# Kernel optimization log

Hardware: AMD Instinct MI355X
Metric: run time of the kernel (lower is better)

The kernel has to match this reference:

```python
import jax, jax.numpy as jnp
import numpy as np

B, P, D = 16, 512, 1024   # batch, num wordpieces, bert_dim (roberta-large)
W, T, E = 400, 32, 64     # num words, num triggers (spans), num entities (spans)
H = 600                   # hidden_num of role_idn_ffn


def _make_idxs(rng, b, m, n, max_len):
    # [start, end) intervals with 0 <= start < end <= n, sorted starts per row
    starts = np.sort(rng.integers(0, n - 1, size=(b, m)), axis=1)
    ends = np.minimum(starts + rng.integers(1, max_len + 1, size=(b, m)), n)
    ends = np.maximum(ends, starts + 1)
    return np.stack([starts, ends], axis=-1).astype(np.int32)


def setup_inputs() -> dict:
    key = jax.random.key(0)
    k1, k2, k3 = jax.random.split(key, 3)
    rng = np.random.default_rng(0)
    return {
        "piece_reprs": jax.random.normal(k1, (B, P, D), dtype=jnp.float32),
        "word_idxs": jnp.asarray(_make_idxs(rng, B, W, P, 4)),
        "trigger_idxs": jnp.asarray(_make_idxs(rng, B, T, W, 8)),
        "entity_idxs": jnp.asarray(_make_idxs(rng, B, E, W, 12)),
        "W0": jax.random.normal(k2, (4 * D, H), dtype=jnp.float32) * 0.02,
        "b0": jnp.zeros((H,), dtype=jnp.float32),
        "W1": jax.random.normal(k3, (H, 2), dtype=jnp.float32) * 0.02,
        "b1": jnp.zeros((2,), dtype=jnp.float32),
    }


def _segment_mean(x, idxs):
    """Mean of x[b, start:end] per interval. x: [B,N,Dm], idxs: [B,M,2] -> [B,M,Dm].
    Vectorized replacement of the nested-loop slice+mean via inclusive prefix sums."""
    cs = jnp.concatenate([jnp.zeros_like(x[:, :1]), jnp.cumsum(x, axis=1)], axis=1)  # [B,N+1,Dm]
    s = jnp.take_along_axis(cs, idxs[:, :, 0:1], axis=1)  # [B,M,Dm]
    e = jnp.take_along_axis(cs, idxs[:, :, 1:2], axis=1)  # [B,M,Dm]
    lens = (idxs[:, :, 1] - idxs[:, :, 0]).astype(x.dtype)[:, :, None]
    return (e - s) / lens


def reference(piece_reprs, word_idxs, trigger_idxs, entity_idxs, W0, b0, W1, b1):
    # encode(): wordpiece -> word averaging (compute_word_reps_avg)
    word_reprs = _segment_mean(piece_reprs, word_idxs)          # [B, W, D]
    # scores(): span mean pooling (compute_span_reprs)
    trig = _segment_mean(word_reprs, trigger_idxs)              # [B, T, D]
    ent = _segment_mean(word_reprs, entity_idxs)                # [B, E, D]
    b, t, d = trig.shape
    e = ent.shape[1]
    # compute_binary_reprs: all (trigger, entity) pairs, trigger index varies slowly
    t_rep = jnp.broadcast_to(trig[:, :, None, :], (b, t, e, d)).reshape(b, t * e, d)
    e_rep = jnp.broadcast_to(ent[:, None, :, :], (b, t, e, d)).reshape(b, t * e, d)
    role = jnp.concatenate([t_rep, e_rep, t_rep * e_rep, jnp.abs(t_rep - e_rep)], axis=-1)  # [B,T*E,4D]
    # role_idn_ffn: Linears([4D, H, 2]) with relu between layers (dropout=0 at eval)
    h = jax.nn.relu(role @ W0 + b0)
    return h @ W1 + b1                                          # [B, T*E, 2]
```

## Files before the change

### kernel.cpp

```cpp
#include <hip/hip_runtime.h>
#include <cstddef>
#include <cstdint>

typedef float f32x4 __attribute__((ext_vector_type(4)));
typedef __bf16 bf16x8 __attribute__((ext_vector_type(8)));

constexpr int NB = 16;
constexpr int NP = 512;
constexpr int ND = 1024;
constexpr int NW = 400;
constexpr int NT = 32;
constexpr int NE = 64;
constexpr int NH = 600;
constexpr int IMGP = 128 * 64;
constexpr int IMGQ = 320 * 32;

__device__ inline bf16x8 pack8(float a0, float a1, float a2, float a3,
                               float a4, float a5, float a6, float a7) {
    bf16x8 v;
    v[0] = (__bf16)a0; v[1] = (__bf16)a1; v[2] = (__bf16)a2; v[3] = (__bf16)a3;
    v[4] = (__bf16)a4; v[5] = (__bf16)a5; v[6] = (__bf16)a6; v[7] = (__bf16)a7;
    return v;
}

__device__ inline void dma16(const void* g, void* l) {
    __builtin_amdgcn_global_load_lds(
        (const __attribute__((address_space(1))) uint32_t*)g,
        (__attribute__((address_space(3))) uint32_t*)l, 16, 0, 0);
}

__global__ __launch_bounds__(256) void word_mean_kernel(
    const float* __restrict__ piece, const int* __restrict__ widx,
    float* __restrict__ word) {
    int bw = blockIdx.x;
    int b = bw / NW;
    int s = widx[bw * 2], e = widx[bw * 2 + 1];
    int col = threadIdx.x * 4;
    const float* base = piece + (size_t)b * NP * ND + col;
    float4 acc = make_float4(0.f, 0.f, 0.f, 0.f);
    for (int r = s; r < e; ++r) {
        float4 v = *(const float4*)(base + (size_t)r * ND);
        acc.x += v.x; acc.y += v.y; acc.z += v.z; acc.w += v.w;
    }
    float inv = 1.0f / (float)(e - s);
    acc.x *= inv; acc.y *= inv; acc.z *= inv; acc.w *= inv;
    *(float4*)(word + (size_t)bw * ND + col) = acc;
}

__global__ __launch_bounds__(256) void span_mean_kernel(
    const float* __restrict__ word, const int* __restrict__ tidx,
    const int* __restrict__ eidx, float* __restrict__ trig,
    float* __restrict__ ent) {
    int id = blockIdx.x;
    const int* idx;
    float* out;
    int b;
    if (id < NB * NT) {
        b = id / NT; idx = tidx + id * 2; out = trig + (size_t)id * ND;
    } else {
        int id2 = id - NB * NT;
        b = id2 / NE; idx = eidx + id2 * 2; out = ent + (size_t)id2 * ND;
    }
    int s = idx[0], e = idx[1];
    int col = threadIdx.x * 4;
    const float* base = word + (size_t)b * NW * ND + col;
    float4 acc = make_float4(0.f, 0.f, 0.f, 0.f);
    for (int r = s; r < e; ++r) {
        float4 v = *(const float4*)(base + (size_t)r * ND);
        acc.x += v.x; acc.y += v.y; acc.z += v.z; acc.w += v.w;
    }
    float inv = 1.0f / (float)(e - s);
    acc.x *= inv; acc.y *= inv; acc.z *= inv; acc.w *= inv;
    *(float4*)(out + col) = acc;
}

__global__ __launch_bounds__(256) void w0_swizzle_kernel(
    const float* __restrict__ W0, __bf16* __restrict__ W0pre) {
    __shared__ float T[64][132];
    int kb = blockIdx.x, nc = blockIdx.y;
    int t = threadIdx.x;
    {
        int kl = t >> 2;
        int n0 = (t & 3) * 32;
        int kg = kb * 64 + kl;
        const float* src = W0 + (size_t)kg * NH + nc * 128 + n0;
#pragma unroll
        for (int g = 0; g < 8; ++g) {
            int n = nc * 128 + n0 + g * 4;
            float4 v = (n < NH) ? *(const float4*)(src + g * 4)
                                : make_float4(0.f, 0.f, 0.f, 0.f);
            *(float4*)&T[kl][n0 + g * 4] = v;
        }
    }
    __syncthreads();
#pragma unroll
    for (int s = 0; s < 4; ++s) {
        int idx = t * 4 + s;
        int row = idx >> 3, c = idx & 7;
        bf16x8 v = pack8(T[c * 8 + 0][row], T[c * 8 + 1][row],
                         T[c * 8 + 2][row], T[c * 8 + 3][row],
                         T[c * 8 + 4][row], T[c * 8 + 5][row],
                         T[c * 8 + 6][row], T[c * 8 + 7][row]);
        __bf16* img = W0pre + ((size_t)nc * 32 + kb) * IMGP;
        *(bf16x8*)&img[row * 64 + ((c ^ (row & 7)) << 3)] = v;
    }
}

__global__ __launch_bounds__(256) void w0_pair_kernel(
    const float* __restrict__ W0, __bf16* __restrict__ W0pair) {
    __shared__ float T[32][84];
    int it = blockIdx.x, nc = blockIdx.y, zz = blockIdx.z;
    int tid = threadIdx.x;
    {
        int kidx = tid >> 3, part = tid & 7;
        int korig = (kidx < 16) ? (2048 + it * 16 + kidx)
                                : (3072 + it * 16 + (kidx - 16));
        const float* src = W0 + (size_t)korig * NH;
#pragma unroll
        for (int g = 0; g < 10; ++g) {
            int n = nc * 320 + zz * 80 + part * 10 + g;
            T[kidx][part * 10 + g] = (n < NH) ? src[n] : 0.0f;
        }
    }
    __syncthreads();
    __bf16* img = W0pair + ((size_t)nc * 64 + it) * IMGQ;
#pragma unroll
    for (int s = 0; s < 2; ++s) {
        int idx = s * 256 + tid;
        if (idx < 320) {
            int rloc = idx >> 2, c = idx & 3;
            bf16x8 v = pack8(T[c * 8 + 0][rloc], T[c * 8 + 1][rloc],
                             T[c * 8 + 2][rloc], T[c * 8 + 3][rloc],
                             T[c * 8 + 4][rloc], T[c * 8 + 5][rloc],
                             T[c * 8 + 6][rloc], T[c * 8 + 7][rloc]);
            int rg = zz * 80 + rloc;
            int slot = ((rg >> 1) + c) & 3;
            *(bf16x8*)&img[rg * 32 + slot * 8] = v;
        }
    }
}

__global__ __launch_bounds__(256) void pre_mfma_kernel(
    const float* __restrict__ trig, const float* __restrict__ ent,
    const __bf16* __restrict__ W0pre, float* __restrict__ pre_t,
    float* __restrict__ pre_e) {
    __shared__ __bf16 As[128 * 64];
    __shared__ __bf16 Bs[128 * 64];
    int mb = blockIdx.x, nc = blockIdx.y;
    const float* A;
    float* C;
    int kbofs, mbase;
    if (mb < 4) { A = trig; C = pre_t; kbofs = 0;  mbase = mb * 128; }
    else        { A = ent;  C = pre_e; kbofs = 16; mbase = (mb - 4) * 128; }
    int tid = threadIdx.x;
    int lane = tid & 63, w = tid >> 6, rw = w & 1, cw = w >> 1;
    int q = lane >> 4, l15 = lane & 15, sa = l15 & 7;
    int ar = tid >> 1, ah = tid & 1;
    const __bf16* imgbase = W0pre + ((size_t)nc * 32 + kbofs) * IMGP;
    f32x4 acc[4][4] = {};

    for (int it = 0; it < 16; ++it) {
        __syncthreads();
        const __bf16* img = imgbase + (size_t)it * IMGP + w * 2048;
#pragma unroll
        for (int i = 0; i < 4; ++i)
            dma16(img + i * 512 + lane * 8, (__bf16*)Bs + w * 2048 + i * 512);
        {
            const float* src = A + (size_t)(mbase + ar) * ND + it * 64 + ah * 32;
#pragma unroll
            for (int i = 0; i < 4; ++i) {
                float4 a0 = *(const float4*)(src + i * 8);
                float4 a1 = *(const float4*)(src + i * 8 + 4);
                int c = ah * 4 + i;
                *(bf16x8*)&As[ar * 64 + ((c ^ (ar & 7)) << 3)] =
                    pack8(a0.x, a0.y, a0.z, a0.w, a1.x, a1.y, a1.z, a1.w);
            }
        }
        __syncthreads();
#pragma unroll
        for (int ks = 0; ks < 2; ++ks) {
            int coff = ((q ^ sa) ^ (ks << 2)) << 3;
            bf16x8 af[4];
#pragma unroll
            for (int mt = 0; mt < 4; ++mt)
                af[mt] = *(const bf16x8*)&As[(64 * rw + 16 * mt + l15) * 64 + coff];
#pragma unroll
            for (int nt = 0; nt < 4; ++nt) {
                bf16x8 bf = *(const bf16x8*)&Bs[(64 * cw + 16 * nt + l15) * 64 + coff];
#pragma unroll
                for (int mt = 0; mt < 4; ++mt)
                    acc[mt][nt] = __builtin_amdgcn_mfma_f32_16x16x32_bf16(
                        af[mt], bf, acc[mt][nt], 0, 0, 0);
            }
        }
    }
#pragma unroll
    for (int mt = 0; mt < 4; ++mt)
#pragma unroll
        for (int r = 0; r < 4; ++r) {
            float* crow =
                C + (size_t)(mbase + 64 * rw + 16 * mt + 4 * q + r) * NH;
#pragma unroll
            for (int nt = 0; nt < 4; ++nt) {
                int n = nc * 128 + 64 * cw + 16 * nt + l15;
                if (n < NH) crow[n] = acc[mt][nt][r];
            }
        }
}

__global__ __launch_bounds__(256, 2) void pair_mfma_kernel(
    const float* __restrict__ trig, const float* __restrict__ ent,
    const __bf16* __restrict__ W0pair, const float* __restrict__ b0,
    const float* __restrict__ pre_t, const float* __restrict__ pre_e,
    const float* __restrict__ W1, const float* __restrict__ b1,
    float* __restrict__ out) {
    __shared__ __bf16 Xs[2][128 * 32];
    __shared__ __bf16 Bs[2][320 * 32];
    __shared__ __bf16 Ts[2048];
    int b = blockIdx.x, tp = blockIdx.y, nc = blockIdx.z;
    int tid = threadIdx.x;
    int lane = tid & 63, w = tid >> 6, rw = w & 1, cw = w >> 1;
    int q = lane >> 4, l15 = lane & 15;
    int xr = tid >> 1, xh = tid & 1;
    const float* t0row = trig + (size_t)(b * NT + tp * 2) * ND;
    const float* erow = ent + (size_t)(b * NE + (xr & 63)) * ND;
    const __bf16* imgbase = W0pair + (size_t)nc * 64 * IMGQ;
    f32x4 acc[4][10] = {};
    float4 ef4[2];

    auto dma_b = [&](int it, int buf) {
        const __bf16* img = imgbase + (size_t)it * IMGQ + w * 2560;
        __bf16* lds = &Bs[buf][w * 2560];
#pragma unroll
        for (int i = 0; i < 5; ++i)
            dma16(img + i * 512 + lane * 8, lds + i * 512);
    };
    auto load_e = [&](int it) {
        const float* er = erow + it * 16 + xh * 8;
        ef4[0] = *(const float4*)er;
        ef4[1] = *(const float4*)(er + 4);
    };
    auto write_x = [&](int it, int buf) {
        bf16x8 tv = *(const bf16x8*)&Ts[(xr >> 6) * 1024 + it * 16 + xh * 8];
        float tf[8], ef[8];
#pragma unroll
        for (int j = 0; j < 8; ++j) tf[j] = (float)tv[j];
        ef[0] = ef4[0].x; ef[1] = ef4[0].y; ef[2] = ef4[0].z; ef[3] = ef4[0].w;
        ef[4] = ef4[1].x; ef[5] = ef4[1].y; ef[6] = ef4[1].z; ef[7] = ef4[1].w;
        int sp = (((xr >> 1) + xh) & 3) * 8;
        int sd = (((xr >> 1) + 2 + xh) & 3) * 8;
        __bf16* xb = &Xs[buf][xr * 32];
        *(bf16x8*)(xb + sp) = pack8(
            tf[0] * ef[0], tf[1] * ef[1], tf[2] * ef[2], tf[3] * ef[3],
            tf[4] * ef[4], tf[5] * ef[5], tf[6] * ef[6], tf[7] * ef[7]);
        *(bf16x8*)(xb + sd) = pack8(
            fabsf(tf[0] - ef[0]), fabsf(tf[1] - ef[1]),
            fabsf(tf[2] - ef[2]), fabsf(tf[3] - ef[3]),
            fabsf(tf[4] - ef[4]), fabsf(tf[5] - ef[5]),
            fabsf(tf[6] - ef[6]), fabsf(tf[7] - ef[7]));
    };
    auto mfma_tile = [&](int buf) {
        const __bf16* X = Xs[buf];
        const __bf16* Bb = Bs[buf];
        bf16x8 af[4];
#pragma unroll
        for (int mt = 0; mt < 4; ++mt) {
            int r = 64 * rw + 16 * mt + l15;
            af[mt] = *(const bf16x8*)&X[r * 32 + (((r >> 1) + q) & 3) * 8];
        }
#pragma unroll
        for (int nt = 0; nt < 10; ++nt) {
            int r = 160 * cw + 16 * nt + l15;
            bf16x8 bv = *(const bf16x8*)&Bb[r * 32 + (((r >> 1) + q) & 3) * 8];
#pragma unroll
            for (int mt = 0; mt < 4; ++mt)
                acc[mt][nt] = __builtin_amdgcn_mfma_f32_16x16x32_bf16(
                    af[mt], bv, acc[mt][nt], 0, 0, 0);
        }
    };

    {
        int k0 = (tid & 127) * 8;
        const float* src = t0row + (tid >> 7) * ND + k0;
        float4 va = *(const float4*)src;
        float4 vb = *(const float4*)(src + 4);
        *(bf16x8*)&Ts[tid * 8] =
            pack8(va.x, va.y, va.z, va.w, vb.x, vb.y, vb.z, vb.w);
    }
    dma_b(0, 0);
    load_e(0);
    __syncthreads();
    write_x(0, 0);
    __syncthreads();

    for (int it = 0; it < 64; ++it) {
        int cur = it & 1, nxt = cur ^ 1;
        if (it < 63) {
            load_e(it + 1);
            dma_b(it + 1, nxt);
        }
        mfma_tile(cur);
        if (it < 63) write_x(it + 1, nxt);
        __syncthreads();
    }

    int tglob = b * NT + tp * 2 + rw;
    const float* preT = pre_t + (size_t)tglob * NH;
    float w10[10], w11[10], b0v[10], ptv[10];
    int nbase = nc * 320 + 160 * cw + l15;
#pragma unroll
    for (int nt = 0; nt < 10; ++nt) {
        int n = nbase + 16 * nt;
        bool v = n < NH;
        w10[nt] = v ? W1[2 * n] : 0.f;
        w11[nt] = v ? W1[2 * n + 1] : 0.f;
        b0v[nt] = v ? b0[n] : 0.f;
        ptv[nt] = v ? preT[n] : 0.f;
    }
    float b10 = b1[0], b11 = b1[1];
    bool lead = (l15 == 0);
    bool addb = (nc == 0) && (cw == 0);
#pragma unroll
    for (int mt = 0; mt < 4; ++mt) {
#pragma unroll
        for (int r = 0; r < 4; ++r) {
            int e = 16 * mt + 4 * q + r;
            const float* preE = pre_e + (size_t)(b * NE + e) * NH;
            float s0 = 0.f, s1 = 0.f;
#pragma unroll
            for (int nt = 0; nt < 10; ++nt) {
                int n = nbase + 16 * nt;
                float pe = (n < NH) ? preE[n] : 0.f;
                float h = acc[mt][nt][r] + ptv[nt] + pe + b0v[nt];
                h = fmaxf(h, 0.f);
                s0 += h * w10[nt];
                s1 += h * w11[nt];
            }
#pragma unroll
            for (int m = 8; m >= 1; m >>= 1) {
                s0 += __shfl_xor(s0, m);
                s1 += __shfl_xor(s1, m);
            }
            if (lead) {
                if (addb) { s0 += b10; s1 += b11; }
                float* o = out + ((size_t)(tglob * NE + e)) * 2;
                atomicAdd(o, s0);
                atomicAdd(o + 1, s1);
            }
        }
    }
}

extern "C" void kernel_launch(void* const* d_in, const int* in_sizes, int n_in,
                              void* d_out, int out_size, void* d_ws,
                              size_t ws_size, hipStream_t stream) {
    const float* piece = (const float*)d_in[0];
    const int* widx = (const int*)d_in[1];
    const int* tidx = (const int*)d_in[2];
    const int* eidx = (const int*)d_in[3];
    const float* W0 = (const float*)d_in[4];
    const float* b0 = (const float*)d_in[5];
    const float* W1 = (const float*)d_in[6];
    const float* b1 = (const float*)d_in[7];
    float* out = (float*)d_out;

    float* ws = (float*)d_ws;
    float* word = ws;
    float* trig = word + (size_t)NB * NW * ND;
    float* ent = trig + (size_t)NB * NT * ND;
    float* pre_t = ent + (size_t)NB * NE * ND;
    float* pre_e = pre_t + (size_t)NB * NT * NH;
    __bf16* W0pre = (__bf16*)word;
    __bf16* W0pair = W0pre + (size_t)5 * 32 * IMGP;

    hipMemsetAsync(d_out, 0, (size_t)out_size * sizeof(float), stream);

    word_mean_kernel<<<NB * NW, 256, 0, stream>>>(piece, widx, word);
    span_mean_kernel<<<NB * (NT + NE), 256, 0, stream>>>(word, tidx, eidx, trig, ent);
    w0_swizzle_kernel<<<dim3(32, 5), 256, 0, stream>>>(W0, W0pre);
    w0_pair_kernel<<<dim3(64, 2, 4), 256, 0, stream>>>(W0, W0pair);
    pre_mfma_kernel<<<dim3(12, 5), 256, 0, stream>>>(trig, ent, W0pre, pre_t, pre_e);
    pair_mfma_kernel<<<dim3(16, 16, 2), 256, 0, stream>>>(
        trig, ent, W0pair, b0, pre_t, pre_e, W1, b1, out);
}
```

Baseline: 251.0 us.

## Merge W0 prep kernels and shrink GEMM tiles to raise grid parallelism

```diff
diff --git a/kernel.cpp b/kernel.cpp
--- a/kernel.cpp
+++ b/kernel.cpp
@@ -13,7 +13,7 @@
 constexpr int NE = 64;
 constexpr int NH = 600;
 constexpr int IMGP = 128 * 64;
-constexpr int IMGQ = 320 * 32;
+constexpr int IMGQ = 160 * 32;
 
 __device__ inline bf16x8 pack8(float a0, float a1, float a2, float a3,
                                float a4, float a5, float a6, float a7) {
@@ -74,68 +74,70 @@
     *(float4*)(out + col) = acc;
 }
 
-__global__ __launch_bounds__(256) void w0_swizzle_kernel(
-    const float* __restrict__ W0, __bf16* __restrict__ W0pre) {
+__global__ __launch_bounds__(256) void w0_build_kernel(
+    const float* __restrict__ W0, __bf16* __restrict__ W0pre,
+    __bf16* __restrict__ W0pair) {
     __shared__ float T[64][132];
-    int kb = blockIdx.x, nc = blockIdx.y;
+    int id = blockIdx.x;
     int t = threadIdx.x;
-    {
-        int kl = t >> 2;
-        int n0 = (t & 3) * 32;
-        int kg = kb * 64 + kl;
-        const float* src = W0 + (size_t)kg * NH + nc * 128 + n0;
-#pragma unroll
-        for (int g = 0; g < 8; ++g) {
-            int n = nc * 128 + n0 + g * 4;
-            float4 v = (n < NH) ? *(const float4*)(src + g * 4)
-                                : make_float4(0.f, 0.f, 0.f, 0.f);
-            *(float4*)&T[kl][n0 + g * 4] = v;
-        }
-    }
-    __syncthreads();
-#pragma unroll
-    for (int s = 0; s < 4; ++s) {
-        int idx = t * 4 + s;
-        int row = idx >> 3, c = idx & 7;
-        bf16x8 v = pack8(T[c * 8 + 0][row], T[c * 8 + 1][row],
-                         T[c * 8 + 2][row], T[c * 8 + 3][row],
-                         T[c * 8 + 4][row], T[c * 8 + 5][row],
-                         T[c * 8 + 6][row], T[c * 8 + 7][row]);
-        __bf16* img = W0pre + ((size_t)nc * 32 + kb) * IMGP;
-        *(bf16x8*)&img[row * 64 + ((c ^ (row & 7)) << 3)] = v;
-    }
-}
-
-__global__ __launch_bounds__(256) void w0_pair_kernel(
-    const float* __restrict__ W0, __bf16* __restrict__ W0pair) {
-    __shared__ float T[32][84];
-    int it = blockIdx.x, nc = blockIdx.y, zz = blockIdx.z;
-    int tid = threadIdx.x;
-    {
-        int kidx = tid >> 3, part = tid & 7;
-        int korig = (kidx < 16) ? (2048 + it * 16 + kidx)
-                                : (3072 + it * 16 + (kidx - 16));
-        const float* src = W0 + (size_t)korig * NH;
-#pragma unroll
-        for (int g = 0; g < 10; ++g) {
-            int n = nc * 320 + zz * 80 + part * 10 + g;
-            T[kidx][part * 10 + g] = (n < NH) ? src[n] : 0.0f;
-        }
-    }
-    __syncthreads();
-    __bf16* img = W0pair + ((size_t)nc * 64 + it) * IMGQ;
-#pragma unroll
-    for (int s = 0; s < 2; ++s) {
-        int idx = s * 256 + tid;
-        if (idx < 320) {
-            int rloc = idx >> 2, c = idx & 3;
-            bf16x8 v = pack8(T[c * 8 + 0][rloc], T[c * 8 + 1][rloc],
-                             T[c * 8 + 2][rloc], T[c * 8 + 3][rloc],
-                             T[c * 8 + 4][rloc], T[c * 8 + 5][rloc],
-                             T[c * 8 + 6][rloc], T[c * 8 + 7][rloc]);
-            int rg = zz * 80 + rloc;
-            int slot = ((rg >> 1) + c) & 3;
-            *(bf16x8*)&img[rg * 32 + slot * 8] = v;
+    if (id < 160) {
+        int kb = id & 31, nc = id >> 5;
+        {
+            int kl = t >> 2;
+            int n0 = (t & 3) * 32;
+            int kg = kb * 64 + kl;
+            const float* src = W0 + (size_t)kg * NH + nc * 128 + n0;
+#pragma unroll
+            for (int g = 0; g < 8; ++g) {
+                int n = nc * 128 + n0 + g * 4;
+                float4 v = (n < NH) ? *(const float4*)(src + g * 4)
+                                    : make_float4(0.f, 0.f, 0.f, 0.f);
+                *(float4*)&T[kl][n0 + g * 4] = v;
+            }
+        }
+        __syncthreads();
+#pragma unroll
+        for (int s = 0; s < 4; ++s) {
+            int idx = t * 4 + s;
+            int row = idx >> 3, c = idx & 7;
+            bf16x8 v = pack8(T[c * 8 + 0][row], T[c * 8 + 1][row],
+                             T[c * 8 + 2][row], T[c * 8 + 3][row],
+                             T[c * 8 + 4][row], T[c * 8 + 5][row],
+                             T[c * 8 + 6][row], T[c * 8 + 7][row]);
+            __bf16* img = W0pre + ((size_t)nc * 32 + kb) * IMGP;
+            *(bf16x8*)&img[row * 64 + ((c ^ (row & 7)) << 3)] = v;
+        }
+    } else {
+        int e = id - 160;
+        int it = e & 63, z = e >> 6;
+        float (*Tp)[164] = reinterpret_cast<float(*)[164]>(&T[0][0]);
+        {
+            int k = t >> 3, seg = t & 7;
+            int korig = (k < 16) ? (2048 + it * 16 + k)
+                                 : (3072 + it * 16 + (k - 16));
+            const float* src = W0 + (size_t)korig * NH;
+#pragma unroll
+            for (int g = 0; g < 5; ++g) {
+                int n = z * 160 + seg * 20 + g * 4;
+                float4 v = (n < NH) ? *(const float4*)(src + n)
+                                    : make_float4(0.f, 0.f, 0.f, 0.f);
+                *(float4*)&Tp[k][seg * 20 + g * 4] = v;
+            }
+        }
+        __syncthreads();
+        __bf16* img = W0pair + ((size_t)z * 64 + it) * IMGQ;
+#pragma unroll
+        for (int s = 0; s < 3; ++s) {
+            int idx = s * 256 + t;
+            if (idx < 640) {
+                int r = idx >> 2, c = idx & 3;
+                bf16x8 v = pack8(Tp[c * 8 + 0][r], Tp[c * 8 + 1][r],
+                                 Tp[c * 8 + 2][r], Tp[c * 8 + 3][r],
+                                 Tp[c * 8 + 4][r], Tp[c * 8 + 5][r],
+                                 Tp[c * 8 + 6][r], Tp[c * 8 + 7][r]);
+                int slot = ((r >> 1) + c) & 3;
+                *(bf16x8*)&img[r * 32 + slot * 8] = v;
+            }
         }
     }
 }
@@ -144,34 +146,38 @@
     const float* __restrict__ trig, const float* __restrict__ ent,
     const __bf16* __restrict__ W0pre, float* __restrict__ pre_t,
     float* __restrict__ pre_e) {
-    __shared__ __bf16 As[128 * 64];
-    __shared__ __bf16 Bs[128 * 64];
-    int mb = blockIdx.x, nc = blockIdx.y;
+    __shared__ __bf16 As[64 * 64];
+    __shared__ __bf16 Bs[64 * 64];
+    int mt8 = blockIdx.x, ntile = blockIdx.y;
     const float* A;
     float* C;
     int kbofs, mbase;
-    if (mb < 4) { A = trig; C = pre_t; kbofs = 0;  mbase = mb * 128; }
-    else        { A = ent;  C = pre_e; kbofs = 16; mbase = (mb - 4) * 128; }
+    if (mt8 < 8) { A = trig; C = pre_t; kbofs = 0;  mbase = mt8 * 64; }
+    else         { A = ent;  C = pre_e; kbofs = 16; mbase = (mt8 - 8) * 64; }
     int tid = threadIdx.x;
     int lane = tid & 63, w = tid >> 6, rw = w & 1, cw = w >> 1;
     int q = lane >> 4, l15 = lane & 15, sa = l15 & 7;
-    int ar = tid >> 1, ah = tid & 1;
-    const __bf16* imgbase = W0pre + ((size_t)nc * 32 + kbofs) * IMGP;
-    f32x4 acc[4][4] = {};
+    int nc = ntile >> 1, half = ntile & 1;
+    const __bf16* imgbase =
+        W0pre + ((size_t)nc * 32 + kbofs) * IMGP + half * 4096;
+    int ar = tid >> 2, seg = tid & 3;
+    f32x4 acc[2][2] = {};
 
     for (int it = 0; it < 16; ++it) {
         __syncthreads();
-        const __bf16* img = imgbase + (size_t)it * IMGP + w * 2048;
-#pragma unroll
-        for (int i = 0; i < 4; ++i)
-            dma16(img + i * 512 + lane * 8, (__bf16*)Bs + w * 2048 + i * 512);
+        const __bf16* img = imgbase + (size_t)it * IMGP;
+#pragma unroll
+        for (int i = 0; i < 2; ++i) {
+            int idx = i * 4 + w;
+            dma16(img + idx * 512 + lane * 8, (__bf16*)Bs + idx * 512);
+        }
         {
-            const float* src = A + (size_t)(mbase + ar) * ND + it * 64 + ah * 32;
-#pragma unroll
-            for (int i = 0; i < 4; ++i) {
-                float4 a0 = *(const float4*)(src + i * 8);
-                float4 a1 = *(const float4*)(src + i * 8 + 4);
-                int c = ah * 4 + i;
+            const float* src = A + (size_t)(mbase + ar) * ND + it * 64;
+#pragma unroll
+            for (int i = 0; i < 2; ++i) {
+                int c = seg * 2 + i;
+                float4 a0 = *(const float4*)(src + c * 8);
+                float4 a1 = *(const float4*)(src + c * 8 + 4);
                 *(bf16x8*)&As[ar * 64 + ((c ^ (ar & 7)) << 3)] =
                     pack8(a0.x, a0.y, a0.z, a0.w, a1.x, a1.y, a1.z, a1.w);
             }
@@ -180,60 +186,63 @@
 #pragma unroll
         for (int ks = 0; ks < 2; ++ks) {
             int coff = ((q ^ sa) ^ (ks << 2)) << 3;
-            bf16x8 af[4];
-#pragma unroll
-            for (int mt = 0; mt < 4; ++mt)
-                af[mt] = *(const bf16x8*)&As[(64 * rw + 16 * mt + l15) * 64 + coff];
-#pragma unroll
-            for (int nt = 0; nt < 4; ++nt) {
-                bf16x8 bf = *(const bf16x8*)&Bs[(64 * cw + 16 * nt + l15) * 64 + coff];
-#pragma unroll
-                for (int mt = 0; mt < 4; ++mt)
+            bf16x8 af[2];
+#pragma unroll
+            for (int mt = 0; mt < 2; ++mt)
+                af[mt] = *(const bf16x8*)&As[(32 * rw + 16 * mt + l15) * 64 + coff];
+#pragma unroll
+            for (int nt = 0; nt < 2; ++nt) {
+                bf16x8 bf = *(const bf16x8*)&Bs[(32 * cw + 16 * nt + l15) * 64 + coff];
+#pragma unroll
+                for (int mt = 0; mt < 2; ++mt)
                     acc[mt][nt] = __builtin_amdgcn_mfma_f32_16x16x32_bf16(
                         af[mt], bf, acc[mt][nt], 0, 0, 0);
             }
         }
     }
 #pragma unroll
-    for (int mt = 0; mt < 4; ++mt)
+    for (int mt = 0; mt < 2; ++mt)
 #pragma unroll
         for (int r = 0; r < 4; ++r) {
             float* crow =
-                C + (size_t)(mbase + 64 * rw + 16 * mt + 4 * q + r) * NH;
-#pragma unroll
-            for (int nt = 0; nt < 4; ++nt) {
-                int n = nc * 128 + 64 * cw + 16 * nt + l15;
+                C + (size_t)(mbase + 32 * rw + 16 * mt + 4 * q + r) * NH;
+#pragma unroll
+            for (int nt = 0; nt < 2; ++nt) {
+                int n = ntile * 64 + 32 * cw + 16 * nt + l15;
                 if (n < NH) crow[n] = acc[mt][nt][r];
             }
         }
 }
 
-__global__ __launch_bounds__(256, 2) void pair_mfma_kernel(
+__global__ __launch_bounds__(256, 4) void pair_mfma_kernel(
     const float* __restrict__ trig, const float* __restrict__ ent,
     const __bf16* __restrict__ W0pair, const float* __restrict__ b0,
     const float* __restrict__ pre_t, const float* __restrict__ pre_e,
     const float* __restrict__ W1, const float* __restrict__ b1,
     float* __restrict__ out) {
     __shared__ __bf16 Xs[2][128 * 32];
-    __shared__ __bf16 Bs[2][320 * 32];
+    __shared__ __bf16 Bs[2][160 * 32];
     __shared__ __bf16 Ts[2048];
-    int b = blockIdx.x, tp = blockIdx.y, nc = blockIdx.z;
+    int b = blockIdx.x, tp = blockIdx.y, z = blockIdx.z;
     int tid = threadIdx.x;
     int lane = tid & 63, w = tid >> 6, rw = w & 1, cw = w >> 1;
     int q = lane >> 4, l15 = lane & 15;
     int xr = tid >> 1, xh = tid & 1;
     const float* t0row = trig + (size_t)(b * NT + tp * 2) * ND;
     const float* erow = ent + (size_t)(b * NE + (xr & 63)) * ND;
-    const __bf16* imgbase = W0pair + (size_t)nc * 64 * IMGQ;
-    f32x4 acc[4][10] = {};
+    const __bf16* imgbase = W0pair + (size_t)z * 64 * IMGQ;
+    f32x4 acc[4][5] = {};
     float4 ef4[2];
 
     auto dma_b = [&](int it, int buf) {
-        const __bf16* img = imgbase + (size_t)it * IMGQ + w * 2560;
-        __bf16* lds = &Bs[buf][w * 2560];
-#pragma unroll
-        for (int i = 0; i < 5; ++i)
-            dma16(img + i * 512 + lane * 8, lds + i * 512);
+        const __bf16* img = imgbase + (size_t)it * IMGQ;
+        __bf16* lds = Bs[buf];
+#pragma unroll
+        for (int i = 0; i < 3; ++i) {
+            int idx = i * 4 + w;
+            if (idx < 10)
+                dma16(img + idx * 512 + lane * 8, lds + idx * 512);
+        }
     };
     auto load_e = [&](int it) {
         const float* er = erow + it * 16 + xh * 8;
@@ -269,8 +278,8 @@
             af[mt] = *(const bf16x8*)&X[r * 32 + (((r >> 1) + q) & 3) * 8];
         }
 #pragma unroll
-        for (int nt = 0; nt < 10; ++nt) {
-            int r = 160 * cw + 16 * nt + l15;
+        for (int nt = 0; nt < 5; ++nt) {
+            int r = 80 * cw + 16 * nt + l15;
             bf16x8 bv = *(const bf16x8*)&Bb[r * 32 + (((r >> 1) + q) & 3) * 8];
 #pragma unroll
             for (int mt = 0; mt < 4; ++mt)
@@ -306,10 +315,10 @@
 
     int tglob = b * NT + tp * 2 + rw;
     const float* preT = pre_t + (size_t)tglob * NH;
-    float w10[10], w11[10], b0v[10], ptv[10];
-    int nbase = nc * 320 + 160 * cw + l15;
-#pragma unroll
-    for (int nt = 0; nt < 10; ++nt) {
+    float w10[5], w11[5], b0v[5], ptv[5];
+    int nbase = z * 160 + 80 * cw + l15;
+#pragma unroll
+    for (int nt = 0; nt < 5; ++nt) {
         int n = nbase + 16 * nt;
         bool v = n < NH;
         w10[nt] = v ? W1[2 * n] : 0.f;
@@ -319,7 +328,7 @@
     }
     float b10 = b1[0], b11 = b1[1];
     bool lead = (l15 == 0);
-    bool addb = (nc == 0) && (cw == 0);
+    bool addb = (z == 0) && (cw == 0);
 #pragma unroll
     for (int mt = 0; mt < 4; ++mt) {
 #pragma unroll
@@ -328,7 +337,7 @@
             const float* preE = pre_e + (size_t)(b * NE + e) * NH;
             float s0 = 0.f, s1 = 0.f;
 #pragma unroll
-            for (int nt = 0; nt < 10; ++nt) {
+            for (int nt = 0; nt < 5; ++nt) {
                 int n = nbase + 16 * nt;
                 float pe = (n < NH) ? preE[n] : 0.f;
                 float h = acc[mt][nt][r] + ptv[nt] + pe + b0v[nt];
@@ -377,9 +386,8 @@
 
     word_mean_kernel<<<NB * NW, 256, 0, stream>>>(piece, widx, word);
     span_mean_kernel<<<NB * (NT + NE), 256, 0, stream>>>(word, tidx, eidx, trig, ent);
-    w0_swizzle_kernel<<<dim3(32, 5), 256, 0, stream>>>(W0, W0pre);
-    w0_pair_kernel<<<dim3(64, 2, 4), 256, 0, stream>>>(W0, W0pair);
-    pre_mfma_kernel<<<dim3(12, 5), 256, 0, stream>>>(trig, ent, W0pre, pre_t, pre_e);
-    pair_mfma_kernel<<<dim3(16, 16, 2), 256, 0, stream>>>(
+    w0_build_kernel<<<416, 256, 0, stream>>>(W0, W0pre, W0pair);
+    pre_mfma_kernel<<<dim3(24, 10), 256, 0, stream>>>(trig, ent, W0pre, pre_t, pre_e);
+    pair_mfma_kernel<<<dim3(16, 16, 4), 256, 0, stream>>>(
         trig, ent, W0pair, b0, pre_t, pre_e, W1, b1, out);
 }
```

Measured after the change: 233.8 us. 1.07x faster.
